# Performance work log

Hardware: AMD Instinct MI355X
Metric: run time of the kernel (lower is better)

Reference implementation:

```python
import jax, jax.numpy as jnp
import numpy as np

N = 20000          # nodes
E = 320000         # edges (avg degree 16)
HID = 256          # hidden_size
HEADS = 8          # num_heads
HD = HID // HEADS  # head_dim = 32


def setup_inputs() -> dict:
    key = jax.random.key(0)
    ks = jax.random.split(key, 12)
    scale = 1.0 / np.sqrt(HID).astype(np.float32)
    def lin_w(k):
        return jax.random.normal(k, (HID, HID), jnp.float32) * scale
    def lin_b(k):
        return jax.random.normal(k, (HID,), jnp.float32) * 0.01
    return {
        "h":   jax.random.normal(ks[0], (N, HID), jnp.float32),
        "Wq": lin_w(ks[1]), "bq": lin_b(ks[2]),
        "Wk": lin_w(ks[3]), "bk": lin_b(ks[4]),
        "Wv": lin_w(ks[5]), "bv": lin_b(ks[6]),
        "Wo": lin_w(ks[7]), "bo": lin_b(ks[8]),
        "rows": jax.random.randint(ks[9],  (E,), 0, N),  # dst/query node of each edge
        "cols": jax.random.randint(ks[10], (E,), 0, N),  # src/key node of each edge
    }


def reference(h, Wq, bq, Wk, bk, Wv, bv, Wo, bo, rows, cols):
    n = h.shape[0]
    scaling = HD ** (-0.5)
    # projections; reshape exactly as torch: (N, head_dim, num_heads)
    q = ((h @ Wq) + bq).reshape(n, HD, HEADS) * scaling
    k = ((h @ Wk) + bk).reshape(n, HD, HEADS)
    v = ((h @ Wv) + bv).reshape(n, HD, HEADS)
    # bsddmm: per-edge, per-head score s[e,h] = sum_d q[rows[e],d,h] * k[cols[e],d,h]
    s = jnp.einsum("edh,edh->eh", q[rows], k[cols])  # [E, HEADS]
    # sparse row-wise softmax (over each row's edges)
    m = jax.ops.segment_max(s, rows, num_segments=n)          # [N, HEADS]
    e = jnp.exp(s - m[rows])                                   # [E, HEADS]
    z = jax.ops.segment_sum(e, rows, num_segments=n)           # [N, HEADS]
    attn = e / z[rows]                                          # [E, HEADS]
    # bspmm: out[i,d,h] = sum_{e: rows[e]=i} attn[e,h] * v[cols[e],d,h]
    out = jax.ops.segment_sum(attn[:, None, :] * v[cols], rows, num_segments=n)  # [N, HD, HEADS]
    return out.reshape(n, -1) @ Wo + bo
```

## Files before the change

kernel.cpp:

```cpp
#include <hip/hip_runtime.h>
#include <hip/hip_bf16.h>
#include <math.h>

#define NNODES 20000
#define NEDGES 320000
#define SCAT_BLOCKS 1250
#define MBLK 313

using f32x4 = __attribute__((ext_vector_type(4))) float;
using s16x8 = __attribute__((ext_vector_type(8))) short;
using u16x8 = __attribute__((ext_vector_type(8))) unsigned short;

__device__ __forceinline__ float bf2f(unsigned short u) {
    union { unsigned int i; float f; } c; c.i = ((unsigned int)u) << 16; return c.f;
}
__device__ __forceinline__ unsigned short f2bf(float f) {
    __hip_bfloat16 h = __float2bfloat16(f);
    return *reinterpret_cast<unsigned short*>(&h);
}
template <int CTRL>
__device__ __forceinline__ float dpp_xadd(float x) {
    union { float f; int i; } a, b;
    a.f = x;
    b.i = __builtin_amdgcn_update_dpp(0, a.i, CTRL, 0xf, 0xf, true);
    return x + b.f;
}

__global__ __launch_bounds__(256) void prep_all_k(
    const float* __restrict__ Wq, const float* __restrict__ bq,
    const float* __restrict__ Wk, const float* __restrict__ bk,
    const float* __restrict__ Wv, const float* __restrict__ bv,
    const float* __restrict__ Wo, const int* __restrict__ rows,
    const float* __restrict__ h,
    unsigned short* __restrict__ wt, float* __restrict__ bp,
    int* __restrict__ counts, unsigned short* __restrict__ hb)
{
    const int gid = blockIdx.x * 256 + threadIdx.x;
    const float SCQ = 0.17677669529663687f * 1.4426950408889634f;
    if (gid < 262144) {
        const int mat = gid >> 16, r = gid & 65535;
        if (mat < 3) {
            const int k = r >> 8, c = r & 255;
            const int n_old = ((c & 31) << 3) | (c >> 5);
            const float* W = (mat == 0) ? Wq : (mat == 1) ? Wk : Wv;
            float val = W[k * 256 + n_old];
            if (mat == 0) val *= SCQ;
            wt[mat * 65536 + c * 256 + k] = f2bf(val);
        } else {
            const int c = r >> 8, n = r & 255;
            const int n_old = ((c & 31) << 3) | (c >> 5);
            wt[3 * 65536 + n * 256 + c] = f2bf(Wo[n_old * 256 + n]);
        }
    } else if (gid < 262912) {
        const int idx = gid - 262144;
        const int mat = idx >> 8, c = idx & 255;
        const int n_old = ((c & 31) << 3) | (c >> 5);
        const float* b = (mat == 0) ? bq : (mat == 1) ? bk : bv;
        float val = b[n_old];
        if (mat == 0) val *= SCQ;
        bp[mat * 256 + c] = val;
    } else if (gid < 582912) {
        atomicAdd(&counts[rows[gid - 262912]], 1);
    } else {
        const int i = (gid - 582912) * 4;
        const float4 f = *reinterpret_cast<const float4*>(&h[i]);
        ushort4 u;
        u.x = f2bf(f.x); u.y = f2bf(f.y); u.z = f2bf(f.z); u.w = f2bf(f.w);
        *reinterpret_cast<ushort4*>(&hb[i]) = u;
    }
}

__global__ __launch_bounds__(1024) void scan_k(const int* __restrict__ counts,
                                               int* __restrict__ row_start)
{
    __shared__ int wsum[16];
    const int t = threadIdx.x, lane = t & 63, w = t >> 6;
    const int base = t * 20;
    int c[20]; int s = 0;
    #pragma unroll
    for (int j = 0; j < 20; ++j) {
        const int idx = base + j;
        c[j] = (idx < NNODES) ? counts[idx] : 0;
        s += c[j];
    }
    int incl = s;
    #pragma unroll
    for (int off = 1; off < 64; off <<= 1) {
        const int y = __shfl_up(incl, off);
        if (lane >= off) incl += y;
    }
    if (lane == 63) wsum[w] = incl;
    __syncthreads();
    int prev = 0;
    for (int i = 0; i < w; ++i) prev += wsum[i];
    int run = prev + incl - s;
    if (t == 0) row_start[0] = 0;
    #pragma unroll
    for (int j = 0; j < 20; ++j) {
        const int idx = base + j;
        run += c[j];
        if (idx < NNODES) row_start[idx + 1] = run;
    }
}

__global__ __launch_bounds__(256) void qkv_scatter_k(
    const unsigned short* __restrict__ hb,
    const unsigned short* __restrict__ wt, const float* __restrict__ bp,
    const int* __restrict__ rows, const int* __restrict__ cols,
    const int* __restrict__ row_start, int* __restrict__ cursor,
    int* __restrict__ cols_sorted,
    unsigned short* __restrict__ qo, unsigned short* __restrict__ ko,
    unsigned short* __restrict__ vo)
{
    const int t = threadIdx.x;
    if (blockIdx.x < SCAT_BLOCKS) {
        const int i = blockIdx.x * 256 + t;
        if (i < NEDGES) {
            const int r = rows[i];
            const int pos = row_start[r] + atomicAdd(&cursor[r], 1);
            cols_sorted[pos] = cols[i];
        }
        return;
    }
    const int gb = blockIdx.x - SCAT_BLOCKS;
    const int bm = (gb % MBLK) * 64;
    const int y = gb / MBLK;
    const int mat = y >> 1;
    const int bn = (y & 1) * 128;
    const unsigned short* W = wt + mat * 65536;
    unsigned short* outp = (mat == 0) ? qo : (mat == 1) ? ko : vo;

    __shared__ __align__(16) unsigned short smem[8448];
#define AS(r, c) smem[(r) * 40 + (c)]
#define BS(r, c) smem[2560 + (r) * 40 + (c)]

    const int lane = t & 63, w = t >> 6;
    const int wr = (w >> 1) * 32, wc = (w & 1) * 64;
    const int l15 = lane & 15, l4 = lane >> 4;

    f32x4 acc[2][4];
    #pragma unroll
    for (int i = 0; i < 2; ++i)
        #pragma unroll
        for (int j = 0; j < 4; ++j) acc[i][j] = (f32x4){0.f, 0.f, 0.f, 0.f};

    const int arow = t >> 2, koff = (t & 3) * 8;
    const int m0 = min(bm + arow, NNODES - 1);
    const unsigned short* pa  = hb + m0 * 256 + koff;
    const unsigned short* pb0 = W + (bn + arow) * 256 + koff;
    const unsigned short* pb1 = W + (bn + arow + 64) * 256 + koff;

    u16x8 ra  = *(const u16x8*)(pa);
    u16x8 rb0 = *(const u16x8*)(pb0);
    u16x8 rb1 = *(const u16x8*)(pb1);

    #pragma unroll
    for (int kt = 0; kt < 8; ++kt) {
        __syncthreads();
        *(u16x8*)&AS(arow, koff)      = ra;
        *(u16x8*)&BS(arow, koff)      = rb0;
        *(u16x8*)&BS(arow + 64, koff) = rb1;
        __syncthreads();
        if (kt < 7) {
            const int k0 = (kt + 1) * 32;
            ra  = *(const u16x8*)(pa + k0);
            rb0 = *(const u16x8*)(pb0 + k0);
            rb1 = *(const u16x8*)(pb1 + k0);
        }
        s16x8 a[2], b[4];
        const int kk = l4 * 8;
        #pragma unroll
        for (int i = 0; i < 2; ++i)
            a[i] = *(const s16x8*)&AS(wr + i * 16 + l15, kk);
        #pragma unroll
        for (int j = 0; j < 4; ++j)
            b[j] = *(const s16x8*)&BS(wc + j * 16 + l15, kk);
        #pragma unroll
        for (int i = 0; i < 2; ++i)
            #pragma unroll
            for (int j = 0; j < 4; ++j)
                acc[i][j] = __builtin_amdgcn_mfma_f32_16x16x32_bf16(a[i], b[j], acc[i][j], 0, 0, 0);
    }
#undef AS
#undef BS

    float bv4[4];
    #pragma unroll
    for (int j = 0; j < 4; ++j) bv4[j] = bp[mat * 256 + bn + wc + j * 16 + l15];
    __syncthreads();
    #pragma unroll
    for (int i = 0; i < 2; ++i)
        #pragma unroll
        for (int r = 0; r < 4; ++r) {
            const int ml = wr + i * 16 + l4 * 4 + r;
            #pragma unroll
            for (int j = 0; j < 4; ++j)
                smem[ml * 132 + wc + j * 16 + l15] = f2bf(acc[i][j][r] + bv4[j]);
        }
    __syncthreads();
    {
        const int orow = t >> 2, ocol = (t & 3) * 32;
        const int m = bm + orow;
        if (m < NNODES) {
            unsigned short* dst = outp + m * 256 + bn + ocol;
            const unsigned short* src = &smem[orow * 132 + ocol];
            #pragma unroll
            for (int s = 0; s < 4; ++s)
                *(u16x8*)(dst + s * 8) = *(const u16x8*)(src + s * 8);
        }
    }
}

__global__ __launch_bounds__(256) void out_mfma_k(
    const unsigned short* __restrict__ A,
    const unsigned short* __restrict__ wt, const float* __restrict__ bo,
    float* __restrict__ C)
{
    const int bm = blockIdx.x * 64;
    const int bn = blockIdx.y * 128;
    const unsigned short* W = wt + 3 * 65536;

    __shared__ __align__(16) unsigned short As[64][40];
    __shared__ __align__(16) unsigned short Bs[128][40];

    const int t = threadIdx.x;
    const int lane = t & 63, w = t >> 6;
    const int wr = (w >> 1) * 32, wc = (w & 1) * 64;
    const int l15 = lane & 15, l4 = lane >> 4;

    f32x4 acc[2][4];
    #pragma unroll
    for (int i = 0; i < 2; ++i)
        #pragma unroll
        for (int j = 0; j < 4; ++j) acc[i][j] = (f32x4){0.f, 0.f, 0.f, 0.f};

    const int arow = t >> 2, koff = (t & 3) * 8;
    const int m0 = min(bm + arow, NNODES - 1);
    const unsigned short* pa  = A + m0 * 256 + koff;
    const unsigned short* pb0 = W + (bn + arow) * 256 + koff;
    const unsigned short* pb1 = W + (bn + arow + 64) * 256 + koff;

    u16x8 ra  = *(const u16x8*)(pa);
    u16x8 rb0 = *(const u16x8*)(pb0);
    u16x8 rb1 = *(const u16x8*)(pb1);

    #pragma unroll
    for (int kt = 0; kt < 8; ++kt) {
        __syncthreads();
        *(u16x8*)&As[arow][koff]      = ra;
        *(u16x8*)&Bs[arow][koff]      = rb0;
        *(u16x8*)&Bs[arow + 64][koff] = rb1;
        __syncthreads();
        if (kt < 7) {
            const int k0 = (kt + 1) * 32;
            ra  = *(const u16x8*)(pa + k0);
            rb0 = *(const u16x8*)(pb0 + k0);
            rb1 = *(const u16x8*)(pb1 + k0);
        }
        s16x8 a[2], b[4];
        const int kk = l4 * 8;
        #pragma unroll
        for (int i = 0; i < 2; ++i)
            a[i] = *(const s16x8*)&As[wr + i * 16 + l15][kk];
        #pragma unroll
        for (int j = 0; j < 4; ++j)
            b[j] = *(const s16x8*)&Bs[wc + j * 16 + l15][kk];
        #pragma unroll
        for (int i = 0; i < 2; ++i)
            #pragma unroll
            for (int j = 0; j < 4; ++j)
                acc[i][j] = __builtin_amdgcn_mfma_f32_16x16x32_bf16(a[i], b[j], acc[i][j], 0, 0, 0);
    }
    #pragma unroll
    for (int i = 0; i < 2; ++i)
        #pragma unroll
        for (int r = 0; r < 4; ++r) {
            const int m = bm + wr + i * 16 + l4 * 4 + r;
            if (m >= NNODES) continue;
            #pragma unroll
            for (int j = 0; j < 4; ++j) {
                const int n = bn + wc + j * 16 + l15;
                C[m * 256 + n] = acc[i][j][r] + bo[n];
            }
        }
}

__global__ __launch_bounds__(256) void row_attn_k(
    const unsigned short* __restrict__ q, const unsigned short* __restrict__ kk_,
    const unsigned short* __restrict__ vv_,
    const int* __restrict__ row_start, const int* __restrict__ cols_sorted,
    unsigned short* __restrict__ ot)
{
    const int lane = threadIdx.x & 63;
    const int w5 = lane & 31;
    const int half = lane >> 5;
    const int row = __builtin_amdgcn_readfirstlane(blockIdx.x * 4 + (threadIdx.x >> 6));
    const int rs = row_start[row];
    const int re = row_start[row + 1];
    const int deg = re - rs;

    float qd[8];
    {
        const u16x8 qu = *reinterpret_cast<const u16x8*>(&q[row * 256 + w5 * 8]);
        #pragma unroll
        for (int d = 0; d < 8; ++d) qd[d] = bf2f(qu[d]);
    }
    float o[8] = {0.f, 0.f, 0.f, 0.f, 0.f, 0.f, 0.f, 0.f};
    float z = 0.f;
    const int* cp = cols_sorted + rs;

#define LP(K, V, base) do { \
    const int c0 = cp[min((base), deg - 1)]; \
    const int c1 = cp[min((base) + 1, deg - 1)]; \
    const int cn = half ? c1 : c0; \
    K = *reinterpret_cast<const u16x8*>(kk_ + cn * 256 + w5 * 8); \
    V = *reinterpret_cast<const u16x8*>(vv_ + cn * 256 + w5 * 8); \
} while (0)

#define CMP(K, V, base) do { \
    float pa_ = qd[0] * bf2f(K[0]); \
    float pb_ = qd[1] * bf2f(K[1]); \
    pa_ = fmaf(qd[2], bf2f(K[2]), pa_); \
    pb_ = fmaf(qd[3], bf2f(K[3]), pb_); \
    pa_ = fmaf(qd[4], bf2f(K[4]), pa_); \
    pb_ = fmaf(qd[5], bf2f(K[5]), pb_); \
    pa_ = fmaf(qd[6], bf2f(K[6]), pa_); \
    pb_ = fmaf(qd[7], bf2f(K[7]), pb_); \
    float p_ = pa_ + pb_; \
    p_ = dpp_xadd<0xB1>(p_); \
    p_ = dpp_xadd<0x4E>(p_); \
    const float e_ = ((base) + half < deg) ? exp2f(p_) : 0.f; \
    z += e_; \
    o[0] = fmaf(e_, bf2f(V[0]), o[0]); \
    o[1] = fmaf(e_, bf2f(V[1]), o[1]); \
    o[2] = fmaf(e_, bf2f(V[2]), o[2]); \
    o[3] = fmaf(e_, bf2f(V[3]), o[3]); \
    o[4] = fmaf(e_, bf2f(V[4]), o[4]); \
    o[5] = fmaf(e_, bf2f(V[5]), o[5]); \
    o[6] = fmaf(e_, bf2f(V[6]), o[6]); \
    o[7] = fmaf(e_, bf2f(V[7]), o[7]); \
} while (0)

    if (deg > 0) {
        u16x8 ak0, av0, ak1, av1, bk0, bv0, bk1, bv1;
        LP(ak0, av0, 0);
        LP(ak1, av1, 2);
        for (int i0 = 0; i0 < deg; i0 += 8) {
            const bool hb2 = (i0 + 4) < deg;
            if (hb2) { LP(bk0, bv0, i0 + 4); LP(bk1, bv1, i0 + 6); }
            CMP(ak0, av0, i0);
            CMP(ak1, av1, i0 + 2);
            if (i0 + 8 < deg) { LP(ak0, av0, i0 + 8); LP(ak1, av1, i0 + 10); }
            if (hb2) { CMP(bk0, bv0, i0 + 4); CMP(bk1, bv1, i0 + 6); }
        }
    }
#undef LP
#undef CMP

    z += __shfl_xor(z, 32);
    #pragma unroll
    for (int d = 0; d < 8; ++d) o[d] += __shfl_xor(o[d], 32);

    if (half == 0) {
        u16x8 r;
        if (deg > 0) {
            const float iz = 1.0f / z;
            #pragma unroll
            for (int d = 0; d < 8; ++d) r[d] = f2bf(o[d] * iz);
        } else {
            #pragma unroll
            for (int d = 0; d < 8; ++d) r[d] = 0;
        }
        *reinterpret_cast<u16x8*>(&ot[row * 256 + w5 * 8]) = r;
    }
}

extern "C" void kernel_launch(void* const* d_in, const int* in_sizes, int n_in,
                              void* d_out, int out_size, void* d_ws, size_t ws_size,
                              hipStream_t stream)
{
    const float* h  = (const float*)d_in[0];
    const float* Wq = (const float*)d_in[1];
    const float* bq = (const float*)d_in[2];
    const float* Wk = (const float*)d_in[3];
    const float* bk = (const float*)d_in[4];
    const float* Wv = (const float*)d_in[5];
    const float* bv = (const float*)d_in[6];
    const float* Wo = (const float*)d_in[7];
    const float* bo = (const float*)d_in[8];
    const int* rows = (const int*)d_in[9];
    const int* cols = (const int*)d_in[10];
    float* outp = (float*)d_out;

    char* ws = (char*)d_ws;
    unsigned short* q_b  = (unsigned short*)(ws + 0);
    unsigned short* k_b  = (unsigned short*)(ws + 10240000);
    unsigned short* v_b  = (unsigned short*)(ws + 20480000);
    unsigned short* ot_b = (unsigned short*)(ws + 30720000);
    unsigned short* h_b  = (unsigned short*)(ws + 40960000);
    unsigned short* wt   = (unsigned short*)(ws + 51200000);
    float* bp            = (float*)(ws + 51724288);
    int* row_start       = (int*)(ws + 51727360);
    int* counts          = (int*)(ws + 51807488);
    int* cursor          = (int*)(ws + 51887488);
    int* cols_sorted     = (int*)(ws + 51967488);

    hipMemsetAsync(ws + 51807488, 0, 160000, stream);

    prep_all_k<<<7277, 256, 0, stream>>>(Wq, bq, Wk, bk, Wv, bv, Wo, rows, h,
                                         wt, bp, counts, h_b);
    scan_k<<<1, 1024, 0, stream>>>(counts, row_start);
    qkv_scatter_k<<<SCAT_BLOCKS + 6 * MBLK, 256, 0, stream>>>(
        h_b, wt, bp, rows, cols, row_start, cursor, cols_sorted, q_b, k_b, v_b);
    row_attn_k<<<5000, 256, 0, stream>>>(q_b, k_b, v_b, row_start, cols_sorted, ot_b);
    out_mfma_k<<<dim3(313, 2), 256, 0, stream>>>(ot_b, wt, bo, outp);
}
```

Before: 215.3 us.

## Merge h conversion into scan kernel, deepen GEMM prefetch and edge-loop unroll

Moves the fp32-to-bf16 conversion of h out of the prep kernel and into extra blocks of the single-block scan kernel, so the scan no longer occupies the GPU alone. Both MFMA GEMM kernels now keep two k-tiles of global loads in flight instead of one. The per-row attention loop processes and prefetches 16 edges per iteration instead of 8. The deeper prefetch and wider unroll raise register pressure, and with an average degree of 16 the wider edge loop may do more masked work on short rows.

```diff
diff --git a/kernel.cpp b/kernel.cpp
--- a/kernel.cpp
+++ b/kernel.cpp
@@ -31,9 +31,8 @@
     const float* __restrict__ Wk, const float* __restrict__ bk,
     const float* __restrict__ Wv, const float* __restrict__ bv,
     const float* __restrict__ Wo, const int* __restrict__ rows,
-    const float* __restrict__ h,
     unsigned short* __restrict__ wt, float* __restrict__ bp,
-    int* __restrict__ counts, unsigned short* __restrict__ hb)
+    int* __restrict__ counts)
 {
     const int gid = blockIdx.x * 256 + threadIdx.x;
     const float SCQ = 0.17677669529663687f * 1.4426950408889634f;
@@ -61,45 +60,48 @@
         bp[mat * 256 + c] = val;
     } else if (gid < 582912) {
         atomicAdd(&counts[rows[gid - 262912]], 1);
+    }
+}
+
+__global__ __launch_bounds__(1024) void scan_hcvt_k(
+    const int* __restrict__ counts, int* __restrict__ row_start,
+    const float* __restrict__ h, unsigned short* __restrict__ hb)
+{
+    if (blockIdx.x == 0) {
+        __shared__ int wsum[16];
+        const int t = threadIdx.x, lane = t & 63, w = t >> 6;
+        const int base = t * 20;
+        int c[20]; int s = 0;
+        #pragma unroll
+        for (int j = 0; j < 20; ++j) {
+            const int idx = base + j;
+            c[j] = (idx < NNODES) ? counts[idx] : 0;
+            s += c[j];
+        }
+        int incl = s;
+        #pragma unroll
+        for (int off = 1; off < 64; off <<= 1) {
+            const int y = __shfl_up(incl, off);
+            if (lane >= off) incl += y;
+        }
+        if (lane == 63) wsum[w] = incl;
+        __syncthreads();
+        int prev = 0;
+        for (int i = 0; i < w; ++i) prev += wsum[i];
+        int run = prev + incl - s;
+        if (t == 0) row_start[0] = 0;
+        #pragma unroll
+        for (int j = 0; j < 20; ++j) {
+            const int idx = base + j;
+            run += c[j];
+            if (idx < NNODES) row_start[idx + 1] = run;
+        }
     } else {
-        const int i = (gid - 582912) * 4;
+        const int i = ((blockIdx.x - 1) * 1024 + threadIdx.x) * 4;
         const float4 f = *reinterpret_cast<const float4*>(&h[i]);
         ushort4 u;
         u.x = f2bf(f.x); u.y = f2bf(f.y); u.z = f2bf(f.z); u.w = f2bf(f.w);
         *reinterpret_cast<ushort4*>(&hb[i]) = u;
-    }
-}
-
-__global__ __launch_bounds__(1024) void scan_k(const int* __restrict__ counts,
-                                               int* __restrict__ row_start)
-{
-    __shared__ int wsum[16];
-    const int t = threadIdx.x, lane = t & 63, w = t >> 6;
-    const int base = t * 20;
-    int c[20]; int s = 0;
-    #pragma unroll
-    for (int j = 0; j < 20; ++j) {
-        const int idx = base + j;
-        c[j] = (idx < NNODES) ? counts[idx] : 0;
-        s += c[j];
-    }
-    int incl = s;
-    #pragma unroll
-    for (int off = 1; off < 64; off <<= 1) {
-        const int y = __shfl_up(incl, off);
-        if (lane >= off) incl += y;
-    }
-    if (lane == 63) wsum[w] = incl;
-    __syncthreads();
-    int prev = 0;
-    for (int i = 0; i < w; ++i) prev += wsum[i];
-    int run = prev + incl - s;
-    if (t == 0) row_start[0] = 0;
-    #pragma unroll
-    for (int j = 0; j < 20; ++j) {
-        const int idx = base + j;
-        run += c[j];
-        if (idx < NNODES) row_start[idx + 1] = run;
     }
 }
 
@@ -150,22 +152,26 @@
     const unsigned short* pb0 = W + (bn + arow) * 256 + koff;
     const unsigned short* pb1 = W + (bn + arow + 64) * 256 + koff;
 
-    u16x8 ra  = *(const u16x8*)(pa);
-    u16x8 rb0 = *(const u16x8*)(pb0);
-    u16x8 rb1 = *(const u16x8*)(pb1);
+    u16x8 ra_c  = *(const u16x8*)(pa);
+    u16x8 rb0_c = *(const u16x8*)(pb0);
+    u16x8 rb1_c = *(const u16x8*)(pb1);
+    u16x8 ra_n  = *(const u16x8*)(pa + 32);
+    u16x8 rb0_n = *(const u16x8*)(pb0 + 32);
+    u16x8 rb1_n = *(const u16x8*)(pb1 + 32);
 
     #pragma unroll
     for (int kt = 0; kt < 8; ++kt) {
         __syncthreads();
-        *(u16x8*)&AS(arow, koff)      = ra;
-        *(u16x8*)&BS(arow, koff)      = rb0;
-        *(u16x8*)&BS(arow + 64, koff) = rb1;
+        *(u16x8*)&AS(arow, koff)      = ra_c;
+        *(u16x8*)&BS(arow, koff)      = rb0_c;
+        *(u16x8*)&BS(arow + 64, koff) = rb1_c;
         __syncthreads();
-        if (kt < 7) {
-            const int k0 = (kt + 1) * 32;
-            ra  = *(const u16x8*)(pa + k0);
-            rb0 = *(const u16x8*)(pb0 + k0);
-            rb1 = *(const u16x8*)(pb1 + k0);
+        ra_c = ra_n; rb0_c = rb0_n; rb1_c = rb1_n;
+        if (kt < 6) {
+            const int k0 = (kt + 2) * 32;
+            ra_n  = *(const u16x8*)(pa + k0);
+            rb0_n = *(const u16x8*)(pb0 + k0);
+            rb1_n = *(const u16x8*)(pb1 + k0);
         }
         s16x8 a[2], b[4];
         const int kk = l4 * 8;
@@ -240,22 +246,26 @@
     const unsigned short* pb0 = W + (bn + arow) * 256 + koff;
     const unsigned short* pb1 = W + (bn + arow + 64) * 256 + koff;
 
-    u16x8 ra  = *(const u16x8*)(pa);
-    u16x8 rb0 = *(const u16x8*)(pb0);
-    u16x8 rb1 = *(const u16x8*)(pb1);
+    u16x8 ra_c  = *(const u16x8*)(pa);
+    u16x8 rb0_c = *(const u16x8*)(pb0);
+    u16x8 rb1_c = *(const u16x8*)(pb1);
+    u16x8 ra_n  = *(const u16x8*)(pa + 32);
+    u16x8 rb0_n = *(const u16x8*)(pb0 + 32);
+    u16x8 rb1_n = *(const u16x8*)(pb1 + 32);
 
     #pragma unroll
     for (int kt = 0; kt < 8; ++kt) {
         __syncthreads();
-        *(u16x8*)&As[arow][koff]      = ra;
-        *(u16x8*)&Bs[arow][koff]      = rb0;
-        *(u16x8*)&Bs[arow + 64][koff] = rb1;
+        *(u16x8*)&As[arow][koff]      = ra_c;
+        *(u16x8*)&Bs[arow][koff]      = rb0_c;
+        *(u16x8*)&Bs[arow + 64][koff] = rb1_c;
         __syncthreads();
-        if (kt < 7) {
-            const int k0 = (kt + 1) * 32;
-            ra  = *(const u16x8*)(pa + k0);
-            rb0 = *(const u16x8*)(pb0 + k0);
-            rb1 = *(const u16x8*)(pb1 + k0);
+        ra_c = ra_n; rb0_c = rb0_n; rb1_c = rb1_n;
+        if (kt < 6) {
+            const int k0 = (kt + 2) * 32;
+            ra_n  = *(const u16x8*)(pa + k0);
+            rb0_n = *(const u16x8*)(pb0 + k0);
+            rb1_n = *(const u16x8*)(pb1 + k0);
         }
         s16x8 a[2], b[4];
         const int kk = l4 * 8;
@@ -342,16 +352,25 @@
 } while (0)
 
     if (deg > 0) {
-        u16x8 ak0, av0, ak1, av1, bk0, bv0, bk1, bv1;
-        LP(ak0, av0, 0);
-        LP(ak1, av1, 2);
-        for (int i0 = 0; i0 < deg; i0 += 8) {
-            const bool hb2 = (i0 + 4) < deg;
-            if (hb2) { LP(bk0, bv0, i0 + 4); LP(bk1, bv1, i0 + 6); }
-            CMP(ak0, av0, i0);
-            CMP(ak1, av1, i0 + 2);
-            if (i0 + 8 < deg) { LP(ak0, av0, i0 + 8); LP(ak1, av1, i0 + 10); }
-            if (hb2) { CMP(bk0, bv0, i0 + 4); CMP(bk1, bv1, i0 + 6); }
+        u16x8 ak0, av0, ak1, av1, ak2, av2, ak3, av3;
+        u16x8 bk0, bv0, bk1, bv1, bk2, bv2, bk3, bv3;
+        LP(ak0, av0, 0); LP(ak1, av1, 2); LP(ak2, av2, 4); LP(ak3, av3, 6);
+        for (int i0 = 0; i0 < deg; i0 += 16) {
+            const bool hb2 = (i0 + 8) < deg;
+            if (hb2) {
+                LP(bk0, bv0, i0 + 8);  LP(bk1, bv1, i0 + 10);
+                LP(bk2, bv2, i0 + 12); LP(bk3, bv3, i0 + 14);
+            }
+            CMP(ak0, av0, i0);     CMP(ak1, av1, i0 + 2);
+            CMP(ak2, av2, i0 + 4); CMP(ak3, av3, i0 + 6);
+            if (i0 + 16 < deg) {
+                LP(ak0, av0, i0 + 16); LP(ak1, av1, i0 + 18);
+                LP(ak2, av2, i0 + 20); LP(ak3, av3, i0 + 22);
+            }
+            if (hb2) {
+                CMP(bk0, bv0, i0 + 8);  CMP(bk1, bv1, i0 + 10);
+                CMP(bk2, bv2, i0 + 12); CMP(bk3, bv3, i0 + 14);
+            }
         }
     }
 #undef LP
@@ -407,9 +426,9 @@
 
     hipMemsetAsync(ws + 51807488, 0, 160000, stream);
 
-    prep_all_k<<<7277, 256, 0, stream>>>(Wq, bq, Wk, bk, Wv, bv, Wo, rows, h,
-                                         wt, bp, counts, h_b);
-    scan_k<<<1, 1024, 0, stream>>>(counts, row_start);
+    prep_all_k<<<2277, 256, 0, stream>>>(Wq, bq, Wk, bk, Wv, bv, Wo, rows,
+                                         wt, bp, counts);
+    scan_hcvt_k<<<1251, 1024, 0, stream>>>(counts, row_start, h, h_b);
     qkv_scatter_k<<<SCAT_BLOCKS + 6 * MBLK, 256, 0, stream>>>(
         h_b, wt, bp, rows, cols, row_start, cursor, cols_sorted, q_b, k_b, v_b);
     row_attn_k<<<5000, 256, 0, stream>>>(q_b, k_b, v_b, row_start, cols_sorted, ot_b);
```

Result: faster. 208.1 us (-3.3%).
